# Optimization experiments

Measured on AMD Instinct MI355X. Metric: run time of the kernel, lower is better.

Reference implementation:

```python
import jax, jax.numpy as jnp
import numpy as np

L = 12        # layer_num
P = 4         # phm_dim
IN_F = 1024   # in_features
OUT_F = 1024  # out_features
R = 1         # phm_rank
IN_P = IN_F // P
OUT_P = OUT_F // P
N = 2 * L * P  # batched kron count


def setup_inputs() -> dict:
    key = jax.random.key(0)
    k1, k2, k3, k4, k5 = jax.random.split(key, 5)
    x = jax.random.normal(k1, (128, IN_F), dtype=jnp.float32)
    W_left_para = jax.random.normal(k2, (2 * L * P * IN_P, R), dtype=jnp.float32) * 0.05
    W_right_para = jax.random.normal(k3, (2 * L * P * R, OUT_P), dtype=jnp.float32) * 0.05
    phm_rule = jax.random.normal(k4, (2 * P * P, P), dtype=jnp.float32) * 0.05
    b = jnp.zeros((2 * L * OUT_F,), dtype=jnp.float32)
    return {"x": x, "W_left_para": W_left_para, "W_right_para": W_right_para,
            "phm_rule": phm_rule, "b": b}


def reference(x, W_left_para, W_right_para, phm_rule, b):
    # Low-rank reconstruction of per-block weights: (N, in_p, out_p)
    Wl = W_left_para.reshape(N, IN_P, R)
    Wr = W_right_para.reshape(N, R, OUT_P)
    W = jnp.einsum('nir,nro->nio', Wl, Wr)
    # phm rule: (2P, P, P) repeated layer_num times along dim 0 -> (N, P, P)
    rule = jnp.tile(phm_rule.reshape(2 * P, P, P), (L, 1, 1))
    # Batched Kronecker product: (N, P*in_p, P*out_p)
    H = jnp.einsum('nij,nkl->nikjl', rule, W).reshape(N, P * IN_P, P * OUT_P)
    # Sum over phm_dim groups: (2L, in_features, out_features)
    H = H.reshape(2 * L, P, IN_F, OUT_F).sum(axis=1)
    # split along dim0 + concat along last dim == transpose-reshape
    H_combined = jnp.transpose(H, (1, 0, 2)).reshape(IN_F, 2 * L * OUT_F)
    y = x @ H_combined + b
    return y
```

## Files before the change

### kernel.cpp

```cpp
#include <hip/hip_runtime.h>

#define LNUM   12
#define PDIM   4
#define IN_F   1024
#define OUT_F  1024
#define IN_P   256
#define OUT_P  256
#define NBLK   96
#define M2L    24
#define OUT_COLS 24576
#define BATCH  128

__global__ __launch_bounds__(256) void phm_fused_kernel(
    const float* __restrict__ x,
    const float* __restrict__ Wl,
    const float* __restrict__ Wr,
    const float* __restrict__ rule,
    const float* __restrict__ b,
    float* __restrict__ out)
{
    __shared__ float4 xs[IN_F / 4];
    __shared__ float  vsm[4][4];

    const int bid  = blockIdx.x;
    const int s    = bid / M2L;
    const int m    = bid - s * M2L;
    const int tid  = threadIdx.x;
    const int w    = tid >> 6;
    const int lane = tid & 63;

    xs[tid] = reinterpret_cast<const float4*>(x + (size_t)s * IN_F)[tid];
    __syncthreads();

    {
        const int n = 4 * m + w;
        const float4 wv = reinterpret_cast<const float4*>(Wl + n * IN_P)[lane];

        float4 a0 = xs[0 * 64 + lane];
        float4 a1 = xs[1 * 64 + lane];
        float4 a2 = xs[2 * 64 + lane];
        float4 a3 = xs[3 * 64 + lane];
        float u0 = a0.x * wv.x + a0.y * wv.y + a0.z * wv.z + a0.w * wv.w;
        float u1 = a1.x * wv.x + a1.y * wv.y + a1.z * wv.z + a1.w * wv.w;
        float u2 = a2.x * wv.x + a2.y * wv.y + a2.z * wv.z + a2.w * wv.w;
        float u3 = a3.x * wv.x + a3.y * wv.y + a3.z * wv.z + a3.w * wv.w;

        #pragma unroll
        for (int mask = 1; mask < 64; mask <<= 1) {
            u0 += __shfl_xor(u0, mask, 64);
            u1 += __shfl_xor(u1, mask, 64);
            u2 += __shfl_xor(u2, mask, 64);
            u3 += __shfl_xor(u3, mask, 64);
        }

        if (lane < 4) {
            const int j = lane;
            const int q = n & 7;
            const float v = rule[(q * 4 + 0) * 4 + j] * u0
                          + rule[(q * 4 + 1) * 4 + j] * u1
                          + rule[(q * 4 + 2) * 4 + j] * u2
                          + rule[(q * 4 + 3) * 4 + j] * u3;
            vsm[w][j] = v;
        }
    }
    __syncthreads();

    {
        const int j = tid >> 6;
        const int l = (tid & 63) * 4;
        const int c = m * OUT_F + j * OUT_P + l;

        float4 acc = reinterpret_cast<const float4*>(b + c)[0];
        #pragma unroll
        for (int p = 0; p < 4; ++p) {
            const float vv = vsm[p][j];
            const float4 wr = reinterpret_cast<const float4*>(Wr + (4 * m + p) * OUT_P + l)[0];
            acc.x += vv * wr.x;
            acc.y += vv * wr.y;
            acc.z += vv * wr.z;
            acc.w += vv * wr.w;
        }
        reinterpret_cast<float4*>(out + (size_t)s * OUT_COLS + c)[0] = acc;
    }
}

extern "C" void kernel_launch(void* const* d_in, const int* in_sizes, int n_in,
                              void* d_out, int out_size, void* d_ws, size_t ws_size,
                              hipStream_t stream) {
    const float* x    = (const float*)d_in[0];
    const float* Wl   = (const float*)d_in[1];
    const float* Wr   = (const float*)d_in[2];
    const float* rule = (const float*)d_in[3];
    const float* b    = (const float*)d_in[4];
    float* out = (float*)d_out;

    dim3 grid(BATCH * M2L);
    dim3 block(256);
    phm_fused_kernel<<<grid, block, 0, stream>>>(x, Wl, Wr, rule, b, out);
}
```

Baseline: 12.10 us.

## Assign one (row, layer) task per wavefront and drop shared memory and barriers

Each wavefront now handles a full (batch row, m) task alone. It loads x directly into registers, computes all four Wl dot products with shuffle reductions, evaluates the rule mixing in registers, and writes all four output segments. This removes the shared-memory staging, both __syncthreads barriers, and the lane<4 serial section, and the grid shrinks to a quarter as many blocks. In exchange each wave does four times the reduction work serially and uses more registers, which can lower latency hiding.

```diff
diff --git a/kernel.cpp b/kernel.cpp
--- a/kernel.cpp
+++ b/kernel.cpp
@@ -19,31 +19,38 @@
     const float* __restrict__ b,
     float* __restrict__ out)
 {
-    __shared__ float4 xs[IN_F / 4];
-    __shared__ float  vsm[4][4];
-
-    const int bid  = blockIdx.x;
-    const int s    = bid / M2L;
-    const int m    = bid - s * M2L;
     const int tid  = threadIdx.x;
     const int w    = tid >> 6;
     const int lane = tid & 63;
+    const int task = blockIdx.x * 4 + w;
+    const int s    = task / M2L;
+    const int m    = task - s * M2L;
 
-    xs[tid] = reinterpret_cast<const float4*>(x + (size_t)s * IN_F)[tid];
-    __syncthreads();
+    const float4* xrow = reinterpret_cast<const float4*>(x + (size_t)s * IN_F);
+    const float4 xa0 = xrow[0 * 64 + lane];
+    const float4 xa1 = xrow[1 * 64 + lane];
+    const float4 xa2 = xrow[2 * 64 + lane];
+    const float4 xa3 = xrow[3 * 64 + lane];
 
-    {
-        const int n = 4 * m + w;
-        const float4 wv = reinterpret_cast<const float4*>(Wl + n * IN_P)[lane];
+    float4 wr[4];
+    #pragma unroll
+    for (int p = 0; p < 4; ++p)
+        wr[p] = reinterpret_cast<const float4*>(Wr + (4 * m + p) * OUT_P)[lane];
+    float4 bv[4];
+    #pragma unroll
+    for (int j = 0; j < 4; ++j)
+        bv[j] = reinterpret_cast<const float4*>(b + m * OUT_F + j * OUT_P)[lane];
 
-        float4 a0 = xs[0 * 64 + lane];
-        float4 a1 = xs[1 * 64 + lane];
-        float4 a2 = xs[2 * 64 + lane];
-        float4 a3 = xs[3 * 64 + lane];
-        float u0 = a0.x * wv.x + a0.y * wv.y + a0.z * wv.z + a0.w * wv.w;
-        float u1 = a1.x * wv.x + a1.y * wv.y + a1.z * wv.z + a1.w * wv.w;
-        float u2 = a2.x * wv.x + a2.y * wv.y + a2.z * wv.z + a2.w * wv.w;
-        float u3 = a3.x * wv.x + a3.y * wv.y + a3.z * wv.z + a3.w * wv.w;
+    float v[4][4];
+    #pragma unroll
+    for (int p = 0; p < 4; ++p) {
+        const int n = 4 * m + p;
+        const float4 wl = reinterpret_cast<const float4*>(Wl + n * IN_P)[lane];
+
+        float u0 = xa0.x * wl.x + xa0.y * wl.y + xa0.z * wl.z + xa0.w * wl.w;
+        float u1 = xa1.x * wl.x + xa1.y * wl.y + xa1.z * wl.z + xa1.w * wl.w;
+        float u2 = xa2.x * wl.x + xa2.y * wl.y + xa2.z * wl.z + xa2.w * wl.w;
+        float u3 = xa3.x * wl.x + xa3.y * wl.y + xa3.z * wl.z + xa3.w * wl.w;
 
         #pragma unroll
         for (int mask = 1; mask < 64; mask <<= 1) {
@@ -53,34 +60,26 @@
             u3 += __shfl_xor(u3, mask, 64);
         }
 
-        if (lane < 4) {
-            const int j = lane;
-            const int q = n & 7;
-            const float v = rule[(q * 4 + 0) * 4 + j] * u0
-                          + rule[(q * 4 + 1) * 4 + j] * u1
-                          + rule[(q * 4 + 2) * 4 + j] * u2
-                          + rule[(q * 4 + 3) * 4 + j] * u3;
-            vsm[w][j] = v;
-        }
+        const int q = n & 7;
+        const float* rq = rule + q * 16;
+        #pragma unroll
+        for (int j = 0; j < 4; ++j)
+            v[p][j] = rq[0 * 4 + j] * u0 + rq[1 * 4 + j] * u1
+                    + rq[2 * 4 + j] * u2 + rq[3 * 4 + j] * u3;
     }
-    __syncthreads();
 
-    {
-        const int j = tid >> 6;
-        const int l = (tid & 63) * 4;
-        const int c = m * OUT_F + j * OUT_P + l;
-
-        float4 acc = reinterpret_cast<const float4*>(b + c)[0];
+    float* orow = out + (size_t)s * OUT_COLS + m * OUT_F;
+    #pragma unroll
+    for (int j = 0; j < 4; ++j) {
+        float4 acc = bv[j];
         #pragma unroll
         for (int p = 0; p < 4; ++p) {
-            const float vv = vsm[p][j];
-            const float4 wr = reinterpret_cast<const float4*>(Wr + (4 * m + p) * OUT_P + l)[0];
-            acc.x += vv * wr.x;
-            acc.y += vv * wr.y;
-            acc.z += vv * wr.z;
-            acc.w += vv * wr.w;
+            acc.x += v[p][j] * wr[p].x;
+            acc.y += v[p][j] * wr[p].y;
+            acc.z += v[p][j] * wr[p].z;
+            acc.w += v[p][j] * wr[p].w;
         }
-        reinterpret_cast<float4*>(out + (size_t)s * OUT_COLS + c)[0] = acc;
+        reinterpret_cast<float4*>(orow + j * OUT_P)[lane] = acc;
     }
 }
 
@@ -94,7 +93,7 @@
     const float* b    = (const float*)d_in[4];
     float* out = (float*)d_out;
 
-    dim3 grid(BATCH * M2L);
+    dim3 grid((BATCH * M2L) / 4);
     dim3 block(256);
     phm_fused_kernel<<<grid, block, 0, stream>>>(x, Wl, Wr, rule, b, out);
 }
```

New measurement: 11.94 us. No clear change (-1.3%).
